# Performance work log

Measured on AMD Instinct MI355X. Metric: run time of the kernel, lower is better.

## Reference

```python
import jax, jax.numpy as jnp
import numpy as np

N_NODES = 100000
N_EDGES = 1600000
NFEAT, NHID, NCLASS = 512, 128, 40


def setup_inputs() -> dict:
    key = jax.random.key(0)
    ks = jax.random.split(key, 8)
    features = jax.random.normal(ks[0], (N_NODES, NFEAT), dtype=jnp.float32)
    edge_src = jax.random.randint(ks[1], (N_EDGES,), 0, N_NODES, dtype=jnp.int32)
    edge_dst = jax.random.randint(ks[2], (N_EDGES,), 0, N_NODES, dtype=jnp.int32)
    edge_weight = jax.random.uniform(ks[3], (N_EDGES,), dtype=jnp.float32)
    W1 = jax.random.normal(ks[4], (NFEAT, NHID), dtype=jnp.float32) * (1.0 / np.sqrt(NFEAT))
    b1 = jnp.zeros((NHID,), dtype=jnp.float32)
    W2 = jax.random.normal(ks[5], (NHID, NCLASS), dtype=jnp.float32) * (1.0 / np.sqrt(NHID))
    b2 = jnp.zeros((NCLASS,), dtype=jnp.float32)
    return {"features": features, "edge_src": edge_src, "edge_dst": edge_dst,
            "edge_weight": edge_weight, "W1": W1, "b1": b1, "W2": W2, "b2": b2}


def _gcn_conv(x, W, b, edge_src, edge_dst, edge_weight, num_nodes):
    # GCNconv: adj @ (x @ W) + b, adj given as weighted edge list (spmm).
    h = x @ W                                   # [N, out]
    msgs = edge_weight[:, None] * h[edge_src]   # [E, out] gather + scale
    agg = jax.ops.segment_sum(msgs, edge_dst, num_segments=num_nodes)  # [N, out]
    return agg + b


def reference(features, edge_src, edge_dst, edge_weight, W1, b1, W2, b2):
    x = _gcn_conv(features, W1, b1, edge_src, edge_dst, edge_weight, N_NODES)
    x = jax.nn.relu(x)
    # dropout is identity in eval mode (deterministic reference)
    x = _gcn_conv(x, W2, b2, edge_src, edge_dst, edge_weight, N_NODES)
    return jax.nn.log_softmax(x, axis=1)
```

## Files before the change

kernel.cpp:

```cpp
#include <hip/hip_runtime.h>
#include <hip/hip_bf16.h>
#include <math.h>

#define N_NODES 100000
#define N_EDGES 1600000
#define NFEAT 512
#define NHID 128
#define NCLASS 40

#define BSH 7
#define BNODES (1 << BSH)
#define NBUCK ((N_NODES + BNODES - 1) / BNODES)

#define PCHUNK 4096
#define PEPT 16
#define PNB ((N_EDGES + PCHUNK - 1) / PCHUNK)

#define CAP 3072
#define KSTG 12

typedef short bf16x8 __attribute__((ext_vector_type(8)));
typedef float f32x4 __attribute__((ext_vector_type(4)));

static __device__ __forceinline__ unsigned short f32_to_bf16(float f) {
    unsigned int u = __float_as_uint(f);
    unsigned int r = u + 0x7FFFu + ((u >> 16) & 1u);
    return (unsigned short)(r >> 16);
}
static __device__ __forceinline__ float bf16_to_f32(unsigned short h) {
    return __uint_as_float(((unsigned int)h) << 16);
}

__global__ __launch_bounds__(256) void bucket_hist_transpose_kernel(
    const int* __restrict__ dst, int* __restrict__ histG,
    const float* __restrict__ W1, unsigned short* __restrict__ Wt, int E)
{
    const int blk = blockIdx.x;
    if (blk >= PNB) {
        int tid2 = (blk - PNB) * 256 + threadIdx.x;
        int n = tid2 >> 9;
        int k = tid2 & 511;
        Wt[tid2] = f32_to_bf16(W1[k * NHID + n]);
        return;
    }
    __shared__ int hl[NBUCK];
    const int t = threadIdx.x;
    for (int j = t; j < NBUCK; j += 256) hl[j] = 0;
    __syncthreads();
    const int c0 = blk * PCHUNK;
    #pragma unroll
    for (int i = 0; i < PEPT; i++) {
        int e = c0 + t + i * 256;
        if (e < E) atomicAdd(&hl[dst[e] >> BSH], 1);
    }
    __syncthreads();
    for (int j = t; j < NBUCK; j += 256) {
        int c = hl[j];
        if (c) atomicAdd(&histG[j * 16], c);
    }
}

__global__ __launch_bounds__(1024) void bucket_scan_kernel(
    const int* __restrict__ histG, int* __restrict__ bofs,
    int* __restrict__ bcursor)
{
    __shared__ int sh[1024];
    const int t = threadIdx.x;
    int v = (t < NBUCK) ? histG[t * 16] : 0;
    sh[t] = v;
    __syncthreads();
    #pragma unroll
    for (int off = 1; off < 1024; off <<= 1) {
        int u = (t >= off) ? sh[t - off] : 0;
        __syncthreads();
        sh[t] += u;
        __syncthreads();
    }
    if (t < NBUCK) {
        int excl = sh[t] - v;
        bofs[t] = excl;
        bcursor[t] = excl;
    }
    if (t == NBUCK - 1) bofs[NBUCK] = sh[t];
}

__global__ __launch_bounds__(256) void partition_kernel(
    const int* __restrict__ src, const int* __restrict__ dst,
    const float* __restrict__ w, int* __restrict__ bcursor,
    int2* __restrict__ sortedA, int E)
{
    __shared__ int hist[NBUCK];
    __shared__ int bbase[NBUCK];
    const int t = threadIdx.x;
    const int c0 = blockIdx.x * PCHUNK;

    for (int j = t; j < NBUCK; j += 256) hist[j] = 0;
    __syncthreads();

    int  myb[PEPT];
    int2 myv[PEPT];
    #pragma unroll
    for (int i = 0; i < PEPT; i++) {
        int e = c0 + t + i * 256;
        if (e < E) {
            int d = dst[e];
            myb[i] = d >> BSH;
            myv[i] = make_int2(src[e] | ((d & (BNODES - 1)) << 17),
                               __float_as_int(w[e]));
            atomicAdd(&hist[myb[i]], 1);
        } else {
            myb[i] = -1;
        }
    }
    __syncthreads();

    for (int j = t; j < NBUCK; j += 256) {
        int c = hist[j];
        bbase[j] = c ? atomicAdd(&bcursor[j], c) : 0;
    }
    __syncthreads();

    #pragma unroll
    for (int i = 0; i < PEPT; i++) {
        if (myb[i] >= 0) {
            int p = atomicAdd(&bbase[myb[i]], 1);
            sortedA[p] = myv[i];
        }
    }
}

__global__ __launch_bounds__(256) void gemm1_mfma_kernel(
    const float* __restrict__ A,
    const unsigned short* __restrict__ Wt,
    unsigned short* __restrict__ h1b,
    int M)
{
    __shared__ unsigned short cstage[4][32 * 130];

    const int tid = threadIdx.x;
    const int w = tid >> 6;
    const int lane = tid & 63;
    const int lr = lane & 15;
    const int quad = lane >> 4;
    const int m0 = blockIdx.x * 128 + w * 32;

    f32x4 acc[2][8];
    #pragma unroll
    for (int rt = 0; rt < 2; rt++)
        #pragma unroll
        for (int ct = 0; ct < 8; ct++)
            acc[rt][ct] = (f32x4){0.f, 0.f, 0.f, 0.f};

    int r0 = m0 + lr;
    int r1 = m0 + 16 + lr;
    int r0c = r0 < M ? r0 : M - 1;
    int r1c = r1 < M ? r1 : M - 1;
    const float* a0p = A + (size_t)r0c * NFEAT + quad * 8;
    const float* a1p = A + (size_t)r1c * NFEAT + quad * 8;
    const unsigned short* bp = Wt + (size_t)lr * NFEAT + quad * 8;

    #pragma unroll 2
    for (int k0 = 0; k0 < NFEAT; k0 += 32) {
        float4 a0a = *(const float4*)(a0p + k0);
        float4 a0b = *(const float4*)(a0p + k0 + 4);
        float4 a1a = *(const float4*)(a1p + k0);
        float4 a1b = *(const float4*)(a1p + k0 + 4);

        bf16x8 fb[8];
        #pragma unroll
        for (int ct = 0; ct < 8; ct++)
            fb[ct] = *(const bf16x8*)(bp + (size_t)ct * 16 * NFEAT + k0);

        bf16x8 fa0, fa1;
        fa0[0] = (short)f32_to_bf16(a0a.x); fa0[1] = (short)f32_to_bf16(a0a.y);
        fa0[2] = (short)f32_to_bf16(a0a.z); fa0[3] = (short)f32_to_bf16(a0a.w);
        fa0[4] = (short)f32_to_bf16(a0b.x); fa0[5] = (short)f32_to_bf16(a0b.y);
        fa0[6] = (short)f32_to_bf16(a0b.z); fa0[7] = (short)f32_to_bf16(a0b.w);
        fa1[0] = (short)f32_to_bf16(a1a.x); fa1[1] = (short)f32_to_bf16(a1a.y);
        fa1[2] = (short)f32_to_bf16(a1a.z); fa1[3] = (short)f32_to_bf16(a1a.w);
        fa1[4] = (short)f32_to_bf16(a1b.x); fa1[5] = (short)f32_to_bf16(a1b.y);
        fa1[6] = (short)f32_to_bf16(a1b.z); fa1[7] = (short)f32_to_bf16(a1b.w);

        #pragma unroll
        for (int ct = 0; ct < 8; ct++) {
            acc[0][ct] = __builtin_amdgcn_mfma_f32_16x16x32_bf16(fa0, fb[ct], acc[0][ct], 0, 0, 0);
            acc[1][ct] = __builtin_amdgcn_mfma_f32_16x16x32_bf16(fa1, fb[ct], acc[1][ct], 0, 0, 0);
        }
    }

    unsigned short* st = cstage[w];
    #pragma unroll
    for (int rt = 0; rt < 2; rt++)
        #pragma unroll
        for (int ct = 0; ct < 8; ct++)
            #pragma unroll
            for (int i = 0; i < 4; i++) {
                int row = rt * 16 + quad * 4 + i;
                int col = ct * 16 + lr;
                st[row * 130 + col] = f32_to_bf16(acc[rt][ct][i]);
            }

    #pragma unroll
    for (int g = 0; g < 8; g++) {
        int row = g * 4 + (lane >> 4);
        int c8 = lane & 15;
        const unsigned short* rp = &st[row * 130 + c8 * 8];
        uint4 v = *(const uint4*)rp;
        int gr = m0 + row;
        if (gr < M)
            *(uint4*)&h1b[(size_t)gr * NHID + c8 * 8] = v;
    }
}

__global__ __launch_bounds__(256) void agg1_gemm2_kernel(
    const int2* __restrict__ sortedA, const int* __restrict__ bofs,
    const unsigned short* __restrict__ h1b, const float* __restrict__ b1,
    const float* __restrict__ W2, float* __restrict__ h2, int N)
{
    __shared__ __align__(16) int2 ebuf[CAP];
    __shared__ int ncnt[BNODES];
    __shared__ int nofs[BNODES];
    __shared__ int ncur[BNODES];
    __shared__ int sc[BNODES];
    __shared__ __align__(16) float xs[8][132];
    __shared__ __align__(16) unsigned short wt2[40 * 132];
    __shared__ float b1s[128];

    const int tid = threadIdx.x;
    const int b = blockIdx.x;
    const int node0 = b << BSH;
    const int nn = min(BNODES, N - node0);
    const int beg = bofs[b];
    const int end = bofs[b + 1];
    const int cnt = end - beg;
    const bool fits = (cnt <= CAP);

    for (int i = tid; i < 40 * 128; i += 256) {
        int c = i >> 7;
        int k = i & 127;
        wt2[c * 132 + k] = f32_to_bf16(W2[k * NCLASS + c]);
    }
    if (tid < 128) b1s[tid] = b1[tid];
    for (int i = tid; i < BNODES; i += 256) ncnt[i] = 0;
    __syncthreads();

    int2 myrec[KSTG];
    if (fits) {
        #pragma unroll
        for (int k = 0; k < KSTG; k++) {
            int i = tid + k * 256;
            if (i < cnt) {
                int2 r = sortedA[beg + i];
                myrec[k] = r;
                atomicAdd(&ncnt[(r.x >> 17) & 127], 1);
            }
        }
        __syncthreads();
        if (tid < 128) sc[tid] = ncnt[tid];
        __syncthreads();
        #pragma unroll
        for (int off = 1; off < 128; off <<= 1) {
            int u = (tid < 128 && tid >= off) ? sc[tid - off] : 0;
            __syncthreads();
            if (tid < 128) sc[tid] += u;
            __syncthreads();
        }
        if (tid < 128) {
            int e0 = sc[tid] - ncnt[tid];
            nofs[tid] = e0;
            ncur[tid] = e0;
        }
        __syncthreads();
        #pragma unroll
        for (int k = 0; k < KSTG; k++) {
            int i = tid + k * 256;
            if (i < cnt) {
                int nd = (myrec[k].x >> 17) & 127;
                int p = atomicAdd(&ncur[nd], 1);
                ebuf[p] = myrec[k];
            }
        }
        __syncthreads();
    }

    const int g = tid >> 5;
    const int lane = tid & 31;
    const unsigned short* hb = h1b + lane * 4;

    for (int it = 0; it < 16; it++) {
        const int ln = it * 8 + g;
        float4 acc = {0.f, 0.f, 0.f, 0.f};
        if (ln < nn) {
            if (fits) {
                const int s0 = nofs[ln];
                const int c0 = ncnt[ln];
                int j = 0;
                for (; j + 8 <= c0; j += 8) {
                    int2 r[8];
                    #pragma unroll
                    for (int q = 0; q < 8; q++) r[q] = ebuf[s0 + j + q];
                    ushort4 hv[8];
                    #pragma unroll
                    for (int q = 0; q < 8; q++)
                        hv[q] = *(const ushort4*)(hb + (size_t)(r[q].x & 0x1FFFF) * NHID);
                    #pragma unroll
                    for (int q = 0; q < 8; q++) {
                        float wj = __int_as_float(r[q].y);
                        acc.x = fmaf(wj, bf16_to_f32(hv[q].x), acc.x);
                        acc.y = fmaf(wj, bf16_to_f32(hv[q].y), acc.y);
                        acc.z = fmaf(wj, bf16_to_f32(hv[q].z), acc.z);
                        acc.w = fmaf(wj, bf16_to_f32(hv[q].w), acc.w);
                    }
                }
                for (; j + 4 <= c0; j += 4) {
                    int2 r[4];
                    #pragma unroll
                    for (int q = 0; q < 4; q++) r[q] = ebuf[s0 + j + q];
                    ushort4 hv[4];
                    #pragma unroll
                    for (int q = 0; q < 4; q++)
                        hv[q] = *(const ushort4*)(hb + (size_t)(r[q].x & 0x1FFFF) * NHID);
                    #pragma unroll
                    for (int q = 0; q < 4; q++) {
                        float wj = __int_as_float(r[q].y);
                        acc.x = fmaf(wj, bf16_to_f32(hv[q].x), acc.x);
                        acc.y = fmaf(wj, bf16_to_f32(hv[q].y), acc.y);
                        acc.z = fmaf(wj, bf16_to_f32(hv[q].z), acc.z);
                        acc.w = fmaf(wj, bf16_to_f32(hv[q].w), acc.w);
                    }
                }
                for (; j < c0; j++) {
                    int2 r = ebuf[s0 + j];
                    float wj = __int_as_float(r.y);
                    ushort4 hv = *(const ushort4*)(hb + (size_t)(r.x & 0x1FFFF) * NHID);
                    acc.x = fmaf(wj, bf16_to_f32(hv.x), acc.x);
                    acc.y = fmaf(wj, bf16_to_f32(hv.y), acc.y);
                    acc.z = fmaf(wj, bf16_to_f32(hv.z), acc.z);
                    acc.w = fmaf(wj, bf16_to_f32(hv.w), acc.w);
                }
            } else {
                for (int e = beg; e < end; e++) {
                    int2 r = sortedA[e];
                    if (((r.x >> 17) & 127) == ln) {
                        float wj = __int_as_float(r.y);
                        ushort4 hv = *(const ushort4*)(hb + (size_t)(r.x & 0x1FFFF) * NHID);
                        acc.x = fmaf(wj, bf16_to_f32(hv.x), acc.x);
                        acc.y = fmaf(wj, bf16_to_f32(hv.y), acc.y);
                        acc.z = fmaf(wj, bf16_to_f32(hv.z), acc.z);
                        acc.w = fmaf(wj, bf16_to_f32(hv.w), acc.w);
                    }
                }
            }
            float4 bb = *(const float4*)&b1s[lane * 4];
            acc.x = fmaxf(acc.x + bb.x, 0.f);
            acc.y = fmaxf(acc.y + bb.y, 0.f);
            acc.z = fmaxf(acc.z + bb.z, 0.f);
            acc.w = fmaxf(acc.w + bb.w, 0.f);
            *(float4*)&xs[g][lane * 4] = acc;
        }
        __syncthreads();

        float* hp = h2 + (size_t)(node0 + it * 8) * NCLASS;
        #pragma unroll
        for (int i = 0; i < 2; i++) {
            int o = tid + i * 256;
            if (o < 8 * NCLASS) {
                int row = o / NCLASS;
                int col = o - row * NCLASS;
                if (it * 8 + row < nn) {
                    const float* ap = &xs[row][0];
                    const unsigned short* wp = &wt2[col * 132];
                    float s = 0.f;
                    #pragma unroll
                    for (int k = 0; k < 128; k += 4) {
                        float4 a4 = *(const float4*)(ap + k);
                        ushort4 w4 = *(const ushort4*)(wp + k);
                        s = fmaf(a4.x, bf16_to_f32(w4.x), s);
                        s = fmaf(a4.y, bf16_to_f32(w4.y), s);
                        s = fmaf(a4.z, bf16_to_f32(w4.z), s);
                        s = fmaf(a4.w, bf16_to_f32(w4.w), s);
                    }
                    hp[o] = s;
                }
            }
        }
        __syncthreads();
    }
}

__global__ __launch_bounds__(256) void agg2_softmax_kernel(
    const int2* __restrict__ sortedA, const int* __restrict__ bofs,
    const float* __restrict__ h2, const float* __restrict__ b2,
    float* __restrict__ out, int N)
{
    __shared__ __align__(16) int2 ebuf[CAP];
    __shared__ int ncnt[BNODES];
    __shared__ int nofs[BNODES];
    __shared__ int ncur[BNODES];
    __shared__ int sc[BNODES];

    const int tid = threadIdx.x;
    const int b = blockIdx.x;
    const int node0 = b << BSH;
    const int nn = min(BNODES, N - node0);
    const int beg = bofs[b];
    const int end = bofs[b + 1];
    const int cnt = end - beg;
    const bool fits = (cnt <= CAP);

    for (int i = tid; i < BNODES; i += 256) ncnt[i] = 0;
    __syncthreads();

    int2 myrec[KSTG];
    if (fits) {
        #pragma unroll
        for (int k = 0; k < KSTG; k++) {
            int i = tid + k * 256;
            if (i < cnt) {
                int2 r = sortedA[beg + i];
                myrec[k] = r;
                atomicAdd(&ncnt[(r.x >> 17) & 127], 1);
            }
        }
        __syncthreads();
        if (tid < 128) sc[tid] = ncnt[tid];
        __syncthreads();
        #pragma unroll
        for (int off = 1; off < 128; off <<= 1) {
            int u = (tid < 128 && tid >= off) ? sc[tid - off] : 0;
            __syncthreads();
            if (tid < 128) sc[tid] += u;
            __syncthreads();
        }
        if (tid < 128) {
            int e0 = sc[tid] - ncnt[tid];
            nofs[tid] = e0;
            ncur[tid] = e0;
        }
        __syncthreads();
        #pragma unroll
        for (int k = 0; k < KSTG; k++) {
            int i = tid + k * 256;
            if (i < cnt) {
                int nd = (myrec[k].x >> 17) & 127;
                int p = atomicAdd(&ncur[nd], 1);
                ebuf[p] = myrec[k];
            }
        }
        __syncthreads();
    }

    const int grp = tid >> 4;
    const int l16 = tid & 15;
    const float* hp0 = h2 + l16 * 4;

    for (int it = 0; it < 8; it++) {
        const int ln = it * 16 + grp;
        float4 acc = {0.f, 0.f, 0.f, 0.f};
        if (ln < nn) {
            if (fits) {
                const int s0 = nofs[ln];
                const int c0 = ncnt[ln];
                int j = 0;
                for (; j + 8 <= c0; j += 8) {
                    int2 r[8];
                    #pragma unroll
                    for (int q = 0; q < 8; q++) r[q] = ebuf[s0 + j + q];
                    if (l16 < 10) {
                        float4 v[8];
                        #pragma unroll
                        for (int q = 0; q < 8; q++)
                            v[q] = *(const float4*)(hp0 + (size_t)(r[q].x & 0x1FFFF) * NCLASS);
                        #pragma unroll
                        for (int q = 0; q < 8; q++) {
                            float wj = __int_as_float(r[q].y);
                            acc.x = fmaf(wj, v[q].x, acc.x);
                            acc.y = fmaf(wj, v[q].y, acc.y);
                            acc.z = fmaf(wj, v[q].z, acc.z);
                            acc.w = fmaf(wj, v[q].w, acc.w);
                        }
                    }
                }
                for (; j + 4 <= c0; j += 4) {
                    int2 r[4];
                    #pragma unroll
                    for (int q = 0; q < 4; q++) r[q] = ebuf[s0 + j + q];
                    if (l16 < 10) {
                        float4 v[4];
                        #pragma unroll
                        for (int q = 0; q < 4; q++)
                            v[q] = *(const float4*)(hp0 + (size_t)(r[q].x & 0x1FFFF) * NCLASS);
                        #pragma unroll
                        for (int q = 0; q < 4; q++) {
                            float wj = __int_as_float(r[q].y);
                            acc.x = fmaf(wj, v[q].x, acc.x);
                            acc.y = fmaf(wj, v[q].y, acc.y);
                            acc.z = fmaf(wj, v[q].z, acc.z);
                            acc.w = fmaf(wj, v[q].w, acc.w);
                        }
                    }
                }
                for (; j < c0; j++) {
                    int2 r = ebuf[s0 + j];
                    if (l16 < 10) {
                        float wj = __int_as_float(r.y);
                        float4 v = *(const float4*)(hp0 + (size_t)(r.x & 0x1FFFF) * NCLASS);
                        acc.x = fmaf(wj, v.x, acc.x);
                        acc.y = fmaf(wj, v.y, acc.y);
                        acc.z = fmaf(wj, v.z, acc.z);
                        acc.w = fmaf(wj, v.w, acc.w);
                    }
                }
            } else {
                for (int e = beg; e < end; e++) {
                    int2 r = sortedA[e];
                    if (((r.x >> 17) & 127) == ln && l16 < 10) {
                        float wj = __int_as_float(r.y);
                        float4 v = *(const float4*)(hp0 + (size_t)(r.x & 0x1FFFF) * NCLASS);
                        acc.x = fmaf(wj, v.x, acc.x);
                        acc.y = fmaf(wj, v.y, acc.y);
                        acc.z = fmaf(wj, v.z, acc.z);
                        acc.w = fmaf(wj, v.w, acc.w);
                    }
                }
            }
        }
        bool act = (ln < nn) && (l16 < 10);
        float mx = -INFINITY;
        if (act) {
            float4 bb = *(const float4*)&b2[l16 * 4];
            acc.x += bb.x; acc.y += bb.y; acc.z += bb.z; acc.w += bb.w;
            mx = fmaxf(fmaxf(acc.x, acc.y), fmaxf(acc.z, acc.w));
        }
        #pragma unroll
        for (int o = 8; o > 0; o >>= 1) mx = fmaxf(mx, __shfl_xor(mx, o, 16));
        float sm = act ? expf(acc.x - mx) + expf(acc.y - mx) +
                         expf(acc.z - mx) + expf(acc.w - mx) : 0.f;
        #pragma unroll
        for (int o = 8; o > 0; o >>= 1) sm += __shfl_xor(sm, o, 16);
        if (act) {
            float l = mx + logf(sm);
            float4 o4 = {acc.x - l, acc.y - l, acc.z - l, acc.w - l};
            *(float4*)&out[(size_t)(node0 + ln) * NCLASS + l16 * 4] = o4;
        }
    }
}

extern "C" void kernel_launch(void* const* d_in, const int* in_sizes, int n_in,
                              void* d_out, int out_size, void* d_ws, size_t ws_size,
                              hipStream_t stream) {
    const float* features = (const float*)d_in[0];
    const int* edge_src   = (const int*)d_in[1];
    const int* edge_dst   = (const int*)d_in[2];
    const float* edge_w   = (const float*)d_in[3];
    const float* W1       = (const float*)d_in[4];
    const float* b1       = (const float*)d_in[5];
    const float* W2       = (const float*)d_in[6];
    const float* b2       = (const float*)d_in[7];
    float* out = (float*)d_out;

    char* base = (char*)d_ws;
    float*          h2       = (float*)base;
    unsigned short* h1b      = (unsigned short*)(base + 51200000);
    unsigned short* Wt       = (unsigned short*)(base + 76800000);
    int*            histG    = (int*)(base + 76931072);
    int*            bofs     = (int*)(base + 77000000);
    int*            bcursor  = (int*)(base + 77010000);
    int2*           sortedA  = (int2*)(base + 90540000);

    hipMemsetAsync(histG, 0, NBUCK * 16 * sizeof(int), stream);

    bucket_hist_transpose_kernel<<<PNB + (NFEAT * NHID) / 256, 256, 0, stream>>>(
        edge_dst, histG, W1, Wt, N_EDGES);
    bucket_scan_kernel<<<1, 1024, 0, stream>>>(histG, bofs, bcursor);
    partition_kernel<<<PNB, 256, 0, stream>>>(
        edge_src, edge_dst, edge_w, bcursor, sortedA, N_EDGES);

    gemm1_mfma_kernel<<<(N_NODES + 127) / 128, 256, 0, stream>>>(features, Wt, h1b, N_NODES);

    agg1_gemm2_kernel<<<NBUCK, 256, 0, stream>>>(
        sortedA, bofs, h1b, b1, W2, h2, N_NODES);

    agg2_softmax_kernel<<<NBUCK, 256, 0, stream>>>(
        sortedA, bofs, h2, b2, out, N_NODES);
}
```

Before: 620.7 us.

## Use MFMA for fused second GEMM and drop per-8-node syncs in agg1

```diff
diff --git a/kernel.cpp b/kernel.cpp
--- a/kernel.cpp
+++ b/kernel.cpp
@@ -16,8 +16,8 @@
 #define PEPT 16
 #define PNB ((N_EDGES + PCHUNK - 1) / PCHUNK)
 
-#define CAP 3072
-#define KSTG 12
+#define CAP 2560
+#define KSTG 10
 
 typedef short bf16x8 __attribute__((ext_vector_type(8)));
 typedef float f32x4 __attribute__((ext_vector_type(4)));
@@ -33,9 +33,19 @@
 
 __global__ __launch_bounds__(256) void bucket_hist_transpose_kernel(
     const int* __restrict__ dst, int* __restrict__ histG,
-    const float* __restrict__ W1, unsigned short* __restrict__ Wt, int E)
+    const float* __restrict__ W1, unsigned short* __restrict__ Wt,
+    const float* __restrict__ W2, unsigned short* __restrict__ W2t, int E)
 {
     const int blk = blockIdx.x;
+    if (blk >= PNB + 256) {
+        int i = (blk - PNB - 256) * 256 + threadIdx.x;
+        if (i < 48 * 128) {
+            int c = i >> 7;
+            int k = i & 127;
+            W2t[i] = (c < NCLASS) ? f32_to_bf16(W2[k * NCLASS + c]) : 0;
+        }
+        return;
+    }
     if (blk >= PNB) {
         int tid2 = (blk - PNB) * 256 + threadIdx.x;
         int n = tid2 >> 9;
@@ -215,15 +225,15 @@
 __global__ __launch_bounds__(256) void agg1_gemm2_kernel(
     const int2* __restrict__ sortedA, const int* __restrict__ bofs,
     const unsigned short* __restrict__ h1b, const float* __restrict__ b1,
-    const float* __restrict__ W2, float* __restrict__ h2, int N)
+    const unsigned short* __restrict__ W2t, float* __restrict__ h2, int N)
 {
     __shared__ __align__(16) int2 ebuf[CAP];
+    __shared__ __align__(16) unsigned short xs[128][136];
+    __shared__ __align__(16) unsigned short wt2s[48 * 136];
     __shared__ int ncnt[BNODES];
     __shared__ int nofs[BNODES];
     __shared__ int ncur[BNODES];
     __shared__ int sc[BNODES];
-    __shared__ __align__(16) float xs[8][132];
-    __shared__ __align__(16) unsigned short wt2[40 * 132];
     __shared__ float b1s[128];
 
     const int tid = threadIdx.x;
@@ -235,13 +245,12 @@
     const int cnt = end - beg;
     const bool fits = (cnt <= CAP);
 
-    for (int i = tid; i < 40 * 128; i += 256) {
-        int c = i >> 7;
-        int k = i & 127;
-        wt2[c * 132 + k] = f32_to_bf16(W2[k * NCLASS + c]);
-    }
-    if (tid < 128) b1s[tid] = b1[tid];
-    for (int i = tid; i < BNODES; i += 256) ncnt[i] = 0;
+    for (int i = tid; i < 48 * 128; i += 256)
+        wt2s[(i >> 7) * 136 + (i & 127)] = W2t[i];
+    if (tid < 128) {
+        b1s[tid] = b1[tid];
+        ncnt[tid] = 0;
+    }
     __syncthreads();
 
     int2 myrec[KSTG];
@@ -287,50 +296,60 @@
     const int lane = tid & 31;
     const unsigned short* hb = h1b + lane * 4;
 
-    for (int it = 0; it < 16; it++) {
-        const int ln = it * 8 + g;
+    for (int ln = g * 16; ln < g * 16 + 16; ln++) {
+        if (ln >= nn) break;
         float4 acc = {0.f, 0.f, 0.f, 0.f};
-        if (ln < nn) {
-            if (fits) {
-                const int s0 = nofs[ln];
-                const int c0 = ncnt[ln];
-                int j = 0;
-                for (; j + 8 <= c0; j += 8) {
-                    int2 r[8];
-                    #pragma unroll
-                    for (int q = 0; q < 8; q++) r[q] = ebuf[s0 + j + q];
-                    ushort4 hv[8];
-                    #pragma unroll
-                    for (int q = 0; q < 8; q++)
-                        hv[q] = *(const ushort4*)(hb + (size_t)(r[q].x & 0x1FFFF) * NHID);
-                    #pragma unroll
-                    for (int q = 0; q < 8; q++) {
-                        float wj = __int_as_float(r[q].y);
-                        acc.x = fmaf(wj, bf16_to_f32(hv[q].x), acc.x);
-                        acc.y = fmaf(wj, bf16_to_f32(hv[q].y), acc.y);
-                        acc.z = fmaf(wj, bf16_to_f32(hv[q].z), acc.z);
-                        acc.w = fmaf(wj, bf16_to_f32(hv[q].w), acc.w);
-                    }
-                }
-                for (; j + 4 <= c0; j += 4) {
-                    int2 r[4];
-                    #pragma unroll
-                    for (int q = 0; q < 4; q++) r[q] = ebuf[s0 + j + q];
-                    ushort4 hv[4];
-                    #pragma unroll
-                    for (int q = 0; q < 4; q++)
-                        hv[q] = *(const ushort4*)(hb + (size_t)(r[q].x & 0x1FFFF) * NHID);
-                    #pragma unroll
-                    for (int q = 0; q < 4; q++) {
-                        float wj = __int_as_float(r[q].y);
-                        acc.x = fmaf(wj, bf16_to_f32(hv[q].x), acc.x);
-                        acc.y = fmaf(wj, bf16_to_f32(hv[q].y), acc.y);
-                        acc.z = fmaf(wj, bf16_to_f32(hv[q].z), acc.z);
-                        acc.w = fmaf(wj, bf16_to_f32(hv[q].w), acc.w);
-                    }
-                }
-                for (; j < c0; j++) {
-                    int2 r = ebuf[s0 + j];
+        if (fits) {
+            const int s0 = nofs[ln];
+            const int c0 = ncnt[ln];
+            int j = 0;
+            for (; j + 8 <= c0; j += 8) {
+                int2 r[8];
+                #pragma unroll
+                for (int q = 0; q < 8; q++) r[q] = ebuf[s0 + j + q];
+                ushort4 hv[8];
+                #pragma unroll
+                for (int q = 0; q < 8; q++)
+                    hv[q] = *(const ushort4*)(hb + (size_t)(r[q].x & 0x1FFFF) * NHID);
+                #pragma unroll
+                for (int q = 0; q < 8; q++) {
+                    float wj = __int_as_float(r[q].y);
+                    acc.x = fmaf(wj, bf16_to_f32(hv[q].x), acc.x);
+                    acc.y = fmaf(wj, bf16_to_f32(hv[q].y), acc.y);
+                    acc.z = fmaf(wj, bf16_to_f32(hv[q].z), acc.z);
+                    acc.w = fmaf(wj, bf16_to_f32(hv[q].w), acc.w);
+                }
+            }
+            for (; j + 4 <= c0; j += 4) {
+                int2 r[4];
+                #pragma unroll
+                for (int q = 0; q < 4; q++) r[q] = ebuf[s0 + j + q];
+                ushort4 hv[4];
+                #pragma unroll
+                for (int q = 0; q < 4; q++)
+                    hv[q] = *(const ushort4*)(hb + (size_t)(r[q].x & 0x1FFFF) * NHID);
+                #pragma unroll
+                for (int q = 0; q < 4; q++) {
+                    float wj = __int_as_float(r[q].y);
+                    acc.x = fmaf(wj, bf16_to_f32(hv[q].x), acc.x);
+                    acc.y = fmaf(wj, bf16_to_f32(hv[q].y), acc.y);
+                    acc.z = fmaf(wj, bf16_to_f32(hv[q].z), acc.z);
+                    acc.w = fmaf(wj, bf16_to_f32(hv[q].w), acc.w);
+                }
+            }
+            for (; j < c0; j++) {
+                int2 r = ebuf[s0 + j];
+                float wj = __int_as_float(r.y);
+                ushort4 hv = *(const ushort4*)(hb + (size_t)(r.x & 0x1FFFF) * NHID);
+                acc.x = fmaf(wj, bf16_to_f32(hv.x), acc.x);
+                acc.y = fmaf(wj, bf16_to_f32(hv.y), acc.y);
+                acc.z = fmaf(wj, bf16_to_f32(hv.z), acc.z);
+                acc.w = fmaf(wj, bf16_to_f32(hv.w), acc.w);
+            }
+        } else {
+            for (int e = beg; e < end; e++) {
+                int2 r = sortedA[e];
+                if (((r.x >> 17) & 127) == ln) {
                     float wj = __int_as_float(r.y);
                     ushort4 hv = *(const ushort4*)(hb + (size_t)(r.x & 0x1FFFF) * NHID);
                     acc.x = fmaf(wj, bf16_to_f32(hv.x), acc.x);
@@ -338,54 +357,61 @@
                     acc.z = fmaf(wj, bf16_to_f32(hv.z), acc.z);
                     acc.w = fmaf(wj, bf16_to_f32(hv.w), acc.w);
                 }
-            } else {
-                for (int e = beg; e < end; e++) {
-                    int2 r = sortedA[e];
-                    if (((r.x >> 17) & 127) == ln) {
-                        float wj = __int_as_float(r.y);
-                        ushort4 hv = *(const ushort4*)(hb + (size_t)(r.x & 0x1FFFF) * NHID);
-                        acc.x = fmaf(wj, bf16_to_f32(hv.x), acc.x);
-                        acc.y = fmaf(wj, bf16_to_f32(hv.y), acc.y);
-                        acc.z = fmaf(wj, bf16_to_f32(hv.z), acc.z);
-                        acc.w = fmaf(wj, bf16_to_f32(hv.w), acc.w);
-                    }
-                }
-            }
-            float4 bb = *(const float4*)&b1s[lane * 4];
-            acc.x = fmaxf(acc.x + bb.x, 0.f);
-            acc.y = fmaxf(acc.y + bb.y, 0.f);
-            acc.z = fmaxf(acc.z + bb.z, 0.f);
-            acc.w = fmaxf(acc.w + bb.w, 0.f);
-            *(float4*)&xs[g][lane * 4] = acc;
-        }
-        __syncthreads();
-
-        float* hp = h2 + (size_t)(node0 + it * 8) * NCLASS;
-        #pragma unroll
-        for (int i = 0; i < 2; i++) {
-            int o = tid + i * 256;
-            if (o < 8 * NCLASS) {
-                int row = o / NCLASS;
-                int col = o - row * NCLASS;
-                if (it * 8 + row < nn) {
-                    const float* ap = &xs[row][0];
-                    const unsigned short* wp = &wt2[col * 132];
-                    float s = 0.f;
-                    #pragma unroll
-                    for (int k = 0; k < 128; k += 4) {
-                        float4 a4 = *(const float4*)(ap + k);
-                        ushort4 w4 = *(const ushort4*)(wp + k);
-                        s = fmaf(a4.x, bf16_to_f32(w4.x), s);
-                        s = fmaf(a4.y, bf16_to_f32(w4.y), s);
-                        s = fmaf(a4.z, bf16_to_f32(w4.z), s);
-                        s = fmaf(a4.w, bf16_to_f32(w4.w), s);
-                    }
-                    hp[o] = s;
-                }
-            }
-        }
-        __syncthreads();
-    }
+            }
+        }
+        float4 bb = *(const float4*)&b1s[lane * 4];
+        ushort4 px;
+        px.x = f32_to_bf16(fmaxf(acc.x + bb.x, 0.f));
+        px.y = f32_to_bf16(fmaxf(acc.y + bb.y, 0.f));
+        px.z = f32_to_bf16(fmaxf(acc.z + bb.z, 0.f));
+        px.w = f32_to_bf16(fmaxf(acc.w + bb.w, 0.f));
+        *(ushort4*)&xs[ln][lane * 4] = px;
+    }
+    __syncthreads();
+
+    const int wv = tid >> 6;
+    const int l64 = tid & 63;
+    const int lr = l64 & 15;
+    const int quad = l64 >> 4;
+
+    f32x4 c_[2][3];
+    #pragma unroll
+    for (int mt = 0; mt < 2; mt++)
+        #pragma unroll
+        for (int nt = 0; nt < 3; nt++)
+            c_[mt][nt] = (f32x4){0.f, 0.f, 0.f, 0.f};
+
+    #pragma unroll
+    for (int k0 = 0; k0 < 128; k0 += 32) {
+        bf16x8 af[2], bf_[3];
+        #pragma unroll
+        for (int mt = 0; mt < 2; mt++)
+            af[mt] = *(const bf16x8*)&xs[wv * 32 + mt * 16 + lr][k0 + quad * 8];
+        #pragma unroll
+        for (int nt = 0; nt < 3; nt++)
+            bf_[nt] = *(const bf16x8*)&wt2s[(nt * 16 + lr) * 136 + k0 + quad * 8];
+        #pragma unroll
+        for (int mt = 0; mt < 2; mt++)
+            #pragma unroll
+            for (int nt = 0; nt < 3; nt++)
+                c_[mt][nt] = __builtin_amdgcn_mfma_f32_16x16x32_bf16(
+                    af[mt], bf_[nt], c_[mt][nt], 0, 0, 0);
+    }
+
+    #pragma unroll
+    for (int mt = 0; mt < 2; mt++)
+        #pragma unroll
+        for (int nt = 0; nt < 3; nt++) {
+            int col = nt * 16 + lr;
+            if (col < NCLASS) {
+                #pragma unroll
+                for (int i = 0; i < 4; i++) {
+                    int row = wv * 32 + mt * 16 + quad * 4 + i;
+                    if (row < nn)
+                        h2[(size_t)(node0 + row) * NCLASS + col] = c_[mt][nt][i];
+                }
+            }
+        }
 }
 
 __global__ __launch_bounds__(256) void agg2_softmax_kernel(
@@ -566,12 +592,13 @@
     int*            histG    = (int*)(base + 76931072);
     int*            bofs     = (int*)(base + 77000000);
     int*            bcursor  = (int*)(base + 77010000);
+    unsigned short* W2t      = (unsigned short*)(base + 77020000);
     int2*           sortedA  = (int2*)(base + 90540000);
 
     hipMemsetAsync(histG, 0, NBUCK * 16 * sizeof(int), stream);
 
-    bucket_hist_transpose_kernel<<<PNB + (NFEAT * NHID) / 256, 256, 0, stream>>>(
-        edge_dst, histG, W1, Wt, N_EDGES);
+    bucket_hist_transpose_kernel<<<PNB + 256 + 24, 256, 0, stream>>>(
+        edge_dst, histG, W1, Wt, W2, W2t, N_EDGES);
     bucket_scan_kernel<<<1, 1024, 0, stream>>>(histG, bofs, bcursor);
     partition_kernel<<<PNB, 256, 0, stream>>>(
         edge_src, edge_dst, edge_w, bcursor, sortedA, N_EDGES);
@@ -579,7 +606,7 @@
     gemm1_mfma_kernel<<<(N_NODES + 127) / 128, 256, 0, stream>>>(features, Wt, h1b, N_NODES);
 
     agg1_gemm2_kernel<<<NBUCK, 256, 0, stream>>>(
-        sortedA, bofs, h1b, b1, W2, h2, N_NODES);
+        sortedA, bofs, h1b, b1, W2t, h2, N_NODES);
 
     agg2_softmax_kernel<<<NBUCK, 256, 0, stream>>>(
         sortedA, bofs, h2, b2, out, N_NODES);
```

Result: faster. 544.9 us (-12.2%).
